# Performance work log

Measured on AMD Instinct MI355X. Metric: run time of the kernel, lower is better.

## Reference

```python
import jax, jax.numpy as jnp
import numpy as np

N = 8192

def setup_inputs() -> dict:
    key = jax.random.key(0)
    adj = jax.random.uniform(key, (N, N), dtype=jnp.float32)  # nonnegative weights
    return {"adj": adj}

def reference(adj) -> jnp.ndarray:
    # Symmetrize: adj + adj_T*(adj_T>adj) - adj*(adj_T>adj) == elementwise max(adj, adj^T)
    a = jnp.maximum(adj, adj.T)
    # Add self-loops: set diagonal to exactly 1 (adj + diag(1 - diag_part(adj)))
    n = a.shape[0]
    eye = jnp.eye(n, dtype=jnp.bool_)
    a = jnp.where(eye, jnp.ones((), a.dtype), a)
    # D^{-1/2} A D^{-1/2}: diag matmuls are equivalent to row/col scaling (O(n^2))
    d_inv_sqrt = jax.lax.rsqrt(jnp.sum(a, axis=1))  # [N]
    return a * d_inv_sqrt[:, None] * d_inv_sqrt[None, :]
```

## Files before the change

### kernel.cpp

```cpp
#include <hip/hip_runtime.h>

#define N 8192
#define T 64
#define TILES (N / T)
#define NPAIRS (TILES * (TILES + 1) / 2)
#define BLOCK 256

__device__ inline void decode_pair(int p, int& bi, int& bj) {
    float t = (float)TILES + 0.5f;
    int g = (int)(t - sqrtf(t * t - 2.0f * (float)p));
    if (g < 0) g = 0;
    if (g > TILES - 1) g = TILES - 1;
    while (g < TILES - 1 && ((g + 1) * TILES - (g + 1) * g / 2) <= p) g++;
    while (g > 0 && (g * TILES - g * (g - 1) / 2) > p) g--;
    bi = g;
    bj = g + (p - (g * TILES - g * (g - 1) / 2));
}


__global__ __launch_bounds__(BLOCK) void k_rowsum(const float* __restrict__ adj,
                                                  float* __restrict__ rowsum) {
    __shared__ float red[T * 17];
    int bi, bj;
    decode_pair((int)blockIdx.x, bi, bj);
    bool diag = (bi == bj);
    int t = threadIdx.x;
    int c4 = t & 15, r4 = t >> 4;

    float4 va[4], vb[4];
    const float* pa = adj + (size_t)(bi * T + 4 * r4) * N + bj * T + 4 * c4;
    #pragma unroll
    for (int x = 0; x < 4; x++) va[x] = *(const float4*)(pa + (size_t)x * N);
    const float* pb = adj + (size_t)(bj * T + 4 * c4) * N + bi * T + 4 * r4;
    #pragma unroll
    for (int y = 0; y < 4; y++) vb[y] = *(const float4*)(pb + (size_t)y * N);

    float rowP[4] = {0.f, 0.f, 0.f, 0.f};
    float colP[4] = {0.f, 0.f, 0.f, 0.f};
    #pragma unroll
    for (int x = 0; x < 4; x++) {
        const float* ax = (const float*)&va[x];
        #pragma unroll
        for (int y = 0; y < 4; y++) {
            float b = ((const float*)&vb[y])[x];
            float m = fmaxf(ax[y], b);
            if (diag && (4 * r4 + x == 4 * c4 + y)) m = 1.0f;
            rowP[x] += m;
            colP[y] += m;
        }
    }

    #pragma unroll
    for (int mask = 1; mask <= 8; mask <<= 1) {
        #pragma unroll
        for (int x = 0; x < 4; x++) rowP[x] += __shfl_xor(rowP[x], mask);
    }
    if (c4 < 4) atomicAdd(&rowsum[bi * T + 4 * r4 + c4], rowP[c4]);

    if (!diag) {
        #pragma unroll
        for (int y = 0; y < 4; y++) red[(4 * c4 + y) * 17 + r4] = colP[y];
        __syncthreads();
        if (t < 64) {
            float s = 0.f;
            #pragma unroll
            for (int k = 0; k < 16; k++) s += red[t * 17 + k];
            atomicAdd(&rowsum[bj * T + t], s);
        }
    }
}

__global__ __launch_bounds__(BLOCK) void k_scale(const float* __restrict__ adj,
                                                 const float* __restrict__ rowsum,
                                                 float* __restrict__ out) {
    int bi, bj;
    decode_pair((int)blockIdx.x, bi, bj);
    bool diag = (bi == bj);
    int t = threadIdx.x;
    int c4 = t & 15, r4 = t >> 4;

    float4 va[4], vb[4];
    const float* pa = adj + (size_t)(bi * T + 4 * r4) * N + bj * T + 4 * c4;
    #pragma unroll
    for (int x = 0; x < 4; x++) va[x] = *(const float4*)(pa + (size_t)x * N);
    const float* pb = adj + (size_t)(bj * T + 4 * c4) * N + bi * T + 4 * r4;
    #pragma unroll
    for (int y = 0; y < 4; y++) vb[y] = *(const float4*)(pb + (size_t)y * N);

    float dA[4], dB[4];
    #pragma unroll
    for (int x = 0; x < 4; x++) dA[x] = rsqrtf(rowsum[bi * T + 4 * r4 + x]);
    #pragma unroll
    for (int y = 0; y < 4; y++) dB[y] = rsqrtf(rowsum[bj * T + 4 * c4 + y]);

    float m[4][4];
    #pragma unroll
    for (int x = 0; x < 4; x++) {
        const float* ax = (const float*)&va[x];
        #pragma unroll
        for (int y = 0; y < 4; y++) {
            float b = ((const float*)&vb[y])[x];
            float v = fmaxf(ax[y], b);
            if (diag && (4 * r4 + x == 4 * c4 + y)) v = 1.0f;
            m[x][y] = v;
        }
    }

    float* po = out + (size_t)(bi * T + 4 * r4) * N + bj * T + 4 * c4;
    #pragma unroll
    for (int x = 0; x < 4; x++) {
        float4 v;
        v.x = m[x][0] * dA[x] * dB[0];
        v.y = m[x][1] * dA[x] * dB[1];
        v.z = m[x][2] * dA[x] * dB[2];
        v.w = m[x][3] * dA[x] * dB[3];
        *(float4*)(po + (size_t)x * N) = v;
    }
    if (!diag) {
        float* pm = out + (size_t)(bj * T + 4 * c4) * N + bi * T + 4 * r4;
        #pragma unroll
        for (int y = 0; y < 4; y++) {
            float4 u;
            u.x = m[0][y] * dB[y] * dA[0];
            u.y = m[1][y] * dB[y] * dA[1];
            u.z = m[2][y] * dB[y] * dA[2];
            u.w = m[3][y] * dB[y] * dA[3];
            *(float4*)(pm + (size_t)y * N) = u;
        }
    }
}

extern "C" void kernel_launch(void* const* d_in, const int* in_sizes, int n_in,
                              void* d_out, int out_size, void* d_ws, size_t ws_size,
                              hipStream_t stream) {
    const float* adj = (const float*)d_in[0];
    float* out = (float*)d_out;
    float* rowsum = (float*)d_ws;

    (void)hipMemsetAsync(rowsum, 0, N * sizeof(float), stream);
    k_rowsum<<<NPAIRS, BLOCK, 0, stream>>>(adj, rowsum);
    k_scale<<<NPAIRS, BLOCK, 0, stream>>>(adj, rowsum, out);
}
```

Measured before the change: 507.6 us.

## Replace rowsum atomics with per-tile partials, add reduction kernel, nontemporal stores

Each tile block now writes its row and column partial sums to a dedicated slot in a TILES×TILES×64 workspace instead of doing atomicAdd into a shared rowsum. A new small kernel reduces the partials per row and computes rsqrt once, so the separate memset is no longer needed. The scale kernel reads precomputed inverse square roots and writes output with nontemporal stores to avoid polluting cache. This removes atomic contention and redundant rsqrt work, but adds a kernel launch and about 4 MB of partial traffic.

```diff
diff --git a/kernel.cpp b/kernel.cpp
--- a/kernel.cpp
+++ b/kernel.cpp
@@ -5,6 +5,8 @@
 #define TILES (N / T)
 #define NPAIRS (TILES * (TILES + 1) / 2)
 #define BLOCK 256
+
+typedef float nfloat4 __attribute__((ext_vector_type(4)));
 
 __device__ inline void decode_pair(int p, int& bi, int& bj) {
     float t = (float)TILES + 0.5f;
@@ -19,7 +21,7 @@
 
 
 __global__ __launch_bounds__(BLOCK) void k_rowsum(const float* __restrict__ adj,
-                                                  float* __restrict__ rowsum) {
+                                                  float* __restrict__ part) {
     __shared__ float red[T * 17];
     int bi, bj;
     decode_pair((int)blockIdx.x, bi, bj);
@@ -55,7 +57,8 @@
         #pragma unroll
         for (int x = 0; x < 4; x++) rowP[x] += __shfl_xor(rowP[x], mask);
     }
-    if (c4 < 4) atomicAdd(&rowsum[bi * T + 4 * r4 + c4], rowP[c4]);
+    float* prow = part + ((size_t)bi * TILES + bj) * T;
+    if (c4 < 4) prow[4 * r4 + c4] = rowP[c4];
 
     if (!diag) {
         #pragma unroll
@@ -65,13 +68,23 @@
             float s = 0.f;
             #pragma unroll
             for (int k = 0; k < 16; k++) s += red[t * 17 + k];
-            atomicAdd(&rowsum[bj * T + t], s);
+            (part + ((size_t)bj * TILES + bi) * T)[t] = s;
         }
     }
 }
 
+__global__ __launch_bounds__(256) void k_dinv(const float* __restrict__ part,
+                                              float* __restrict__ dinv) {
+    int i = (int)blockIdx.x * 256 + (int)threadIdx.x;
+    int a = i >> 6, r = i & 63;
+    float s = 0.f;
+    #pragma unroll 8
+    for (int b = 0; b < TILES; b++) s += part[((size_t)a * TILES + b) * T + r];
+    dinv[i] = rsqrtf(s);
+}
+
 __global__ __launch_bounds__(BLOCK) void k_scale(const float* __restrict__ adj,
-                                                 const float* __restrict__ rowsum,
+                                                 const float* __restrict__ dinv,
                                                  float* __restrict__ out) {
     int bi, bj;
     decode_pair((int)blockIdx.x, bi, bj);
@@ -89,9 +102,9 @@
 
     float dA[4], dB[4];
     #pragma unroll
-    for (int x = 0; x < 4; x++) dA[x] = rsqrtf(rowsum[bi * T + 4 * r4 + x]);
+    for (int x = 0; x < 4; x++) dA[x] = dinv[bi * T + 4 * r4 + x];
     #pragma unroll
-    for (int y = 0; y < 4; y++) dB[y] = rsqrtf(rowsum[bj * T + 4 * c4 + y]);
+    for (int y = 0; y < 4; y++) dB[y] = dinv[bj * T + 4 * c4 + y];
 
     float m[4][4];
     #pragma unroll
@@ -109,23 +122,23 @@
     float* po = out + (size_t)(bi * T + 4 * r4) * N + bj * T + 4 * c4;
     #pragma unroll
     for (int x = 0; x < 4; x++) {
-        float4 v;
-        v.x = m[x][0] * dA[x] * dB[0];
-        v.y = m[x][1] * dA[x] * dB[1];
-        v.z = m[x][2] * dA[x] * dB[2];
-        v.w = m[x][3] * dA[x] * dB[3];
-        *(float4*)(po + (size_t)x * N) = v;
+        nfloat4 v;
+        v[0] = m[x][0] * dA[x] * dB[0];
+        v[1] = m[x][1] * dA[x] * dB[1];
+        v[2] = m[x][2] * dA[x] * dB[2];
+        v[3] = m[x][3] * dA[x] * dB[3];
+        __builtin_nontemporal_store(v, (nfloat4*)(po + (size_t)x * N));
     }
     if (!diag) {
         float* pm = out + (size_t)(bj * T + 4 * c4) * N + bi * T + 4 * r4;
         #pragma unroll
         for (int y = 0; y < 4; y++) {
-            float4 u;
-            u.x = m[0][y] * dB[y] * dA[0];
-            u.y = m[1][y] * dB[y] * dA[1];
-            u.z = m[2][y] * dB[y] * dA[2];
-            u.w = m[3][y] * dB[y] * dA[3];
-            *(float4*)(pm + (size_t)y * N) = u;
+            nfloat4 u;
+            u[0] = m[0][y] * dB[y] * dA[0];
+            u[1] = m[1][y] * dB[y] * dA[1];
+            u[2] = m[2][y] * dB[y] * dA[2];
+            u[3] = m[3][y] * dB[y] * dA[3];
+            __builtin_nontemporal_store(u, (nfloat4*)(pm + (size_t)y * N));
         }
     }
 }
@@ -135,9 +148,10 @@
                               hipStream_t stream) {
     const float* adj = (const float*)d_in[0];
     float* out = (float*)d_out;
-    float* rowsum = (float*)d_ws;
+    float* part = (float*)d_ws;
+    float* dinv = part + (size_t)TILES * TILES * T;
 
-    (void)hipMemsetAsync(rowsum, 0, N * sizeof(float), stream);
-    k_rowsum<<<NPAIRS, BLOCK, 0, stream>>>(adj, rowsum);
-    k_scale<<<NPAIRS, BLOCK, 0, stream>>>(adj, rowsum, out);
+    k_rowsum<<<NPAIRS, BLOCK, 0, stream>>>(adj, part);
+    k_dinv<<<N / 256, 256, 0, stream>>>(part, dinv);
+    k_scale<<<NPAIRS, BLOCK, 0, stream>>>(adj, dinv, out);
 }
```

Measured after the change: 501.5 us. No clear change (-1.2%).
